# Performance work log

Hardware: AMD Instinct MI355X
Metric: run time of the kernel (lower is better)

Reference implementation:

```python
import jax, jax.numpy as jnp
import numpy as np

B, A, C, G = 16, 65472, 81, 50
POS_THRESH = 0.5        # positive_threshold
NEG_POS_RATIO = 3
CENTER_VAR, SIZE_VAR = 0.1, 0.2   # standard SSD encoding variances
BETA = 1.0 / 9


def _make_boxes(key, shape):
    # random valid corner-form boxes in [0,1]
    k1, k2 = jax.random.split(key)
    cxy = jax.random.uniform(k1, shape + (2,), minval=0.1, maxval=0.9)
    wh = jax.random.uniform(k2, shape + (2,), minval=0.05, maxval=0.3)
    lo = jnp.clip(cxy - wh / 2, 0.0, 1.0)
    hi = jnp.clip(cxy + wh / 2, 0.0, 1.0)
    return jnp.concatenate([lo, hi], axis=-1).astype(jnp.float32)


def setup_inputs() -> dict:
    key = jax.random.key(0)
    ks = jax.random.split(key, 6)
    confidence = jax.random.normal(ks[0], (B, A, C), dtype=jnp.float32)
    predicted_locations = jax.random.normal(ks[1], (B, A, 4), dtype=jnp.float32)
    boxes = _make_boxes(ks[2], (B, G))
    labels = jax.random.randint(ks[3], (B, G, 1), 1, C).astype(jnp.float32)
    gts = jnp.concatenate([boxes, labels], axis=-1)          # (B, G, 5)
    counts = jax.random.randint(ks[4], (B,), 1, G + 1)       # valid gt per image
    anchors = _make_boxes(ks[5], (A,))                        # corner form
    return {"confidence": confidence, "predicted_locations": predicted_locations,
            "gts": gts, "counts": counts, "anchors": anchors}


def _center_form(b):
    # corner (x1,y1,x2,y2) -> center (cx,cy,w,h)
    return jnp.concatenate([(b[..., :2] + b[..., 2:]) * 0.5,
                            b[..., 2:] - b[..., :2]], axis=-1)


def _iou(a, b):
    # a: (A,4), b: (G,4), corner form -> (A,G)
    lt = jnp.maximum(a[:, None, :2], b[None, :, :2])
    rb = jnp.minimum(a[:, None, 2:], b[None, :, 2:])
    wh = jnp.clip(rb - lt, 0.0)
    inter = wh[..., 0] * wh[..., 1]
    area_a = (a[:, 2] - a[:, 0]) * (a[:, 3] - a[:, 1])
    area_b = (b[:, 2] - b[:, 0]) * (b[:, 3] - b[:, 1])
    return inter / (area_a[:, None] + area_b[None, :] - inter + 1e-10)


def _encode(matched, anchors_c):
    m = _center_form(matched)
    g_cxcy = (m[..., :2] - anchors_c[..., :2]) / (anchors_c[..., 2:] * CENTER_VAR)
    g_wh = jnp.log(m[..., 2:] / anchors_c[..., 2:] + 1e-10) / SIZE_VAR
    return jnp.concatenate([g_cxcy, g_wh], axis=-1)


def _match(gt, count, anchors, anchors_c):
    # gt: (G,5), count: scalar int
    boxes = gt[:, :4]
    glabels = gt[:, 4].astype(jnp.int32)
    valid = jnp.arange(boxes.shape[0]) < count
    ious = jnp.where(valid[None, :], _iou(anchors, boxes), -1.0)  # (A,G)
    best_iou = ious.max(axis=1)          # best gt per anchor
    best_idx = ious.argmax(axis=1)
    best_anchor = ious.argmax(axis=0)    # best anchor per gt (G,)
    # force-match: each valid gt claims its best anchor (invalid -> dropped)
    scat = jnp.where(valid, best_anchor, anchors.shape[0])
    best_idx = best_idx.at[scat].set(jnp.arange(boxes.shape[0]), mode='drop')
    best_iou = best_iou.at[scat].set(2.0, mode='drop')
    labels = jnp.where(best_iou < POS_THRESH, 0, glabels[best_idx])  # (A,)
    loc = _encode(boxes[best_idx], anchors_c)                         # (A,4)
    return labels, loc


def reference(confidence, predicted_locations, gts, counts, anchors):
    anchors_c = _center_form(anchors)
    labels, gt_locations = jax.vmap(
        lambda g, c: _match(g, c, anchors, anchors_c))(gts, counts)
    labels = jax.lax.stop_gradient(labels)
    gt_locations = jax.lax.stop_gradient(gt_locations)

    logp = jax.nn.log_softmax(confidence, axis=2)          # (B,A,C)
    pos_mask = labels > 0
    num_pos_b = pos_mask.sum(axis=1)                        # (B,)

    # hard negative mining on background loss (positives excluded via -inf)
    mining = jnp.where(pos_mask, -jnp.inf, jax.lax.stop_gradient(-logp[:, :, 0]))
    order = jnp.argsort(-mining, axis=1)   # descending
    rank = jnp.argsort(order, axis=1)
    neg_mask = rank < (NEG_POS_RATIO * num_pos_b)[:, None]
    mask = pos_mask | neg_mask

    num_pos = jnp.maximum(1.0, pos_mask.sum().astype(jnp.float32))

    # masked cross-entropy (sum) == F.cross_entropy(conf[mask], labels[mask], 'sum')
    ce = -jnp.take_along_axis(logp, labels[..., None], axis=2)[..., 0]
    classification_loss = jnp.sum(jnp.where(mask, ce, 0.0)) / (num_pos * 4.0)

    # smooth L1 over positive anchors only
    n = jnp.abs(predicted_locations - gt_locations)
    sl1 = jnp.where(n < BETA, 0.5 * n * n / BETA, n - 0.5 * BETA)
    localisation_loss = jnp.sum(jnp.where(pos_mask[..., None], sl1, 0.0)) / (num_pos * 4.0)
    return (localisation_loss, classification_loss)
```

## Files before the change

### kernel.cpp

```cpp
#include <hip/hip_runtime.h>
#include <math.h>

#define Bn 16
#define An 65472
#define Cn 81
#define Gn 50
#define ROWS 128
#define NBUCK 1024
#define LISTCAP 8192

static_assert((Bn * (long long)An) % ROWS == 0, "rows divide");

constexpr float POS_THRESH_C = 0.5f;
constexpr float BETA_C = 1.0f / 9.0f;

typedef const __attribute__((address_space(1))) void GPTR;
typedef __attribute__((address_space(3))) void LPTR;

__global__ __launch_bounds__(64) void k0_zero(int* __restrict__ numpos_b,
                                              float* __restrict__ fsums) {
    int t = threadIdx.x;
    if (t < Bn) numpos_b[t] = 0;
    if (t == 32) fsums[0] = 0.f;
    if (t == 33) fsums[1] = 0.f;
}

__global__ __launch_bounds__(256) void k0b_zero(int* __restrict__ ghist) {
    ghist[blockIdx.x * 256 + threadIdx.x] = 0;
}

__global__ __launch_bounds__(256) void k1a(const float* __restrict__ anchors,
                                           const float* __restrict__ gts,
                                           const int* __restrict__ counts,
                                           float* __restrict__ best_iou,
                                           int* __restrict__ best_idx) {
    const int b = blockIdx.y;
    __shared__ float sg[Gn * 5];
    const int t = threadIdx.x;
    if (t < Gn * 5) sg[t] = gts[b * Gn * 5 + t];
    __syncthreads();
    const int a = blockIdx.x * 256 + t;
    if (a >= An) return;
    const int cnt = counts[b];
    const float4 av = ((const float4*)anchors)[a];
    const float area_a = (av.z - av.x) * (av.w - av.y);
    float best = -1.0f;
    int bidx = 0;
    for (int g = 0; g < Gn; ++g) {
        if (g >= cnt) break;
        const float bx0 = sg[g * 5 + 0], by0 = sg[g * 5 + 1];
        const float bx1 = sg[g * 5 + 2], by1 = sg[g * 5 + 3];
        const float w = fmaxf(fminf(av.z, bx1) - fmaxf(av.x, bx0), 0.f);
        const float h = fmaxf(fminf(av.w, by1) - fmaxf(av.y, by0), 0.f);
        const float inter = w * h;
        const float area_b = (bx1 - bx0) * (by1 - by0);
        const float iou = inter / (area_a + area_b - inter + 1e-10f);
        if (iou > best) { best = iou; bidx = g; }
    }
    best_iou[(size_t)b * An + a] = best;
    best_idx[(size_t)b * An + a] = bidx;
}

__global__ __launch_bounds__(256) void k1b(const float* __restrict__ anchors,
                                           const float* __restrict__ gts,
                                           const int* __restrict__ counts,
                                           int* __restrict__ best_anchor) {
    const int b = blockIdx.y, g = blockIdx.x;
    const int t = threadIdx.x;
    const int cnt = counts[b];
    if (g >= cnt) { if (t == 0) best_anchor[b * Gn + g] = 0; return; }
    const float bx0 = gts[(b * Gn + g) * 5 + 0], by0 = gts[(b * Gn + g) * 5 + 1];
    const float bx1 = gts[(b * Gn + g) * 5 + 2], by1 = gts[(b * Gn + g) * 5 + 3];
    const float area_b = (bx1 - bx0) * (by1 - by0);
    const float4* a4 = (const float4*)anchors;
    float best = -2.f;
    int bidx = 0x7fffffff;
    for (int base = t; base < An; base += 1024) {
        const int a1 = base + 256, a2 = base + 512, a3 = base + 768;
        const float4 av0 = a4[base];
        float4 av1, av2, av3;
        const bool ok1 = a1 < An, ok2 = a2 < An, ok3 = a3 < An;
        if (ok1) av1 = a4[a1];
        if (ok2) av2 = a4[a2];
        if (ok3) av3 = a4[a3];
        {
            const float area_a = (av0.z - av0.x) * (av0.w - av0.y);
            const float w = fmaxf(fminf(av0.z, bx1) - fmaxf(av0.x, bx0), 0.f);
            const float h = fmaxf(fminf(av0.w, by1) - fmaxf(av0.y, by0), 0.f);
            const float inter = w * h;
            const float iou = inter / (area_a + area_b - inter + 1e-10f);
            if (iou > best) { best = iou; bidx = base; }
        }
        if (ok1) {
            const float area_a = (av1.z - av1.x) * (av1.w - av1.y);
            const float w = fmaxf(fminf(av1.z, bx1) - fmaxf(av1.x, bx0), 0.f);
            const float h = fmaxf(fminf(av1.w, by1) - fmaxf(av1.y, by0), 0.f);
            const float inter = w * h;
            const float iou = inter / (area_a + area_b - inter + 1e-10f);
            if (iou > best) { best = iou; bidx = a1; }
        }
        if (ok2) {
            const float area_a = (av2.z - av2.x) * (av2.w - av2.y);
            const float w = fmaxf(fminf(av2.z, bx1) - fmaxf(av2.x, bx0), 0.f);
            const float h = fmaxf(fminf(av2.w, by1) - fmaxf(av2.y, by0), 0.f);
            const float inter = w * h;
            const float iou = inter / (area_a + area_b - inter + 1e-10f);
            if (iou > best) { best = iou; bidx = a2; }
        }
        if (ok3) {
            const float area_a = (av3.z - av3.x) * (av3.w - av3.y);
            const float w = fmaxf(fminf(av3.z, bx1) - fmaxf(av3.x, bx0), 0.f);
            const float h = fmaxf(fminf(av3.w, by1) - fmaxf(av3.y, by0), 0.f);
            const float inter = w * h;
            const float iou = inter / (area_a + area_b - inter + 1e-10f);
            if (iou > best) { best = iou; bidx = a3; }
        }
    }
    __shared__ float rv[256];
    __shared__ int ri[256];
    rv[t] = best; ri[t] = bidx;
    __syncthreads();
    for (int s = 128; s > 0; s >>= 1) {
        if (t < s) {
            const float fv = rv[t + s]; const int fi = ri[t + s];
            if (fv > rv[t] || (fv == rv[t] && fi < ri[t])) { rv[t] = fv; ri[t] = fi; }
        }
        __syncthreads();
    }
    if (t == 0) best_anchor[b * Gn + g] = ri[0];
}

__global__ __launch_bounds__(64) void k1c(const int* __restrict__ counts,
                                          const int* __restrict__ best_anchor,
                                          float* __restrict__ best_iou,
                                          int* __restrict__ best_idx) {
    const int b = threadIdx.x;
    if (b >= Bn) return;
    const int cnt = counts[b] < Gn ? counts[b] : Gn;
    for (int g = 0; g < cnt; ++g) {
        const int a = best_anchor[b * Gn + g];
        best_idx[(size_t)b * An + a] = g;
        best_iou[(size_t)b * An + a] = 2.0f;
    }
}

__global__ __launch_bounds__(256) void k2(const float* __restrict__ conf,
                                          const float* __restrict__ pred,
                                          const float* __restrict__ gts,
                                          const float* __restrict__ anchors,
                                          const float* __restrict__ best_iou,
                                          const int* __restrict__ best_idx,
                                          int* __restrict__ v_int,
                                          int* __restrict__ numpos_b,
                                          float* __restrict__ fsums) {
    __shared__ __align__(16) float sc[ROWS * Cn];
    __shared__ float s_ce[4], s_loc[4];
    __shared__ int s_n0[4], s_n1[4];
    const int t = threadIdx.x;
    {
        const float* gp = conf + (size_t)blockIdx.x * (ROWS * Cn);
#pragma unroll
        for (int k = 0; k < 10; ++k) {
            const int c = k * 256 + t;
            __builtin_amdgcn_global_load_lds((GPTR*)(gp + c * 4), (LPTR*)(sc + c * 4), 16, 0, 0);
        }
        if (t < 32) {
            const int c = 2560 + t;
            __builtin_amdgcn_global_load_lds((GPTR*)(gp + c * 4), (LPTR*)(sc + c * 4), 16, 0, 0);
        }
    }
    __syncthreads();
    const int r = t >> 1, h = t & 1;
    const float* row = sc + r * Cn;
    const int j0 = h ? 41 : 0;
    const int j1 = h ? Cn : 41;
    float s0 = 0.f, s1 = 0.f;
    for (int j = j0; j + 1 < j1; j += 2) { s0 += __expf(row[j]); s1 += __expf(row[j + 1]); }
    if (((j1 - j0) & 1) != 0) s0 += __expf(row[j1 - 1]);
    const float s = s0 + s1;
    const float S = s + __shfl_xor(s, 1);
    const float lse = logf(S);

    float ce = 0.f, loc = 0.f;
    int n0 = 0, n1 = 0;
    const int bf = (int)(((size_t)blockIdx.x * ROWS) / An);
    if (h == 0) {
        const size_t gidx = (size_t)blockIdx.x * ROWS + r;
        const int b = (int)(gidx / An);
        const int a = (int)(gidx - (size_t)b * An);
        const float bi = best_iou[gidx];
        const int idx = best_idx[gidx];
        if (bi < POS_THRESH_C) {
            v_int[gidx] = __float_as_int(lse - row[0]);
        } else {
            v_int[gidx] = -1;
            int lab = (int)gts[((size_t)b * Gn + idx) * 5 + 4];
            lab = lab < 0 ? 0 : (lab > Cn - 1 ? Cn - 1 : lab);
            ce = lse - row[lab];
            if (b == bf) n0 = 1; else n1 = 1;
            const float bx0 = gts[((size_t)b * Gn + idx) * 5 + 0];
            const float by0 = gts[((size_t)b * Gn + idx) * 5 + 1];
            const float bx1 = gts[((size_t)b * Gn + idx) * 5 + 2];
            const float by1 = gts[((size_t)b * Gn + idx) * 5 + 3];
            const float4 av = ((const float4*)anchors)[a];
            const float acx = (av.x + av.z) * 0.5f, acy = (av.y + av.w) * 0.5f;
            const float aw = av.z - av.x, ah = av.w - av.y;
            float tt[4];
            tt[0] = ((bx0 + bx1) * 0.5f - acx) / (aw * 0.1f);
            tt[1] = ((by0 + by1) * 0.5f - acy) / (ah * 0.1f);
            tt[2] = logf((bx1 - bx0) / aw + 1e-10f) / 0.2f;
            tt[3] = logf((by1 - by0) / ah + 1e-10f) / 0.2f;
            const float4 p = ((const float4*)pred)[gidx];
            const float pk[4] = {p.x, p.y, p.z, p.w};
#pragma unroll
            for (int k = 0; k < 4; ++k) {
                const float n = fabsf(pk[k] - tt[k]);
                loc += (n < BETA_C) ? 0.5f * n * n / BETA_C : n - 0.5f * BETA_C;
            }
        }
    }
#pragma unroll
    for (int off = 32; off > 0; off >>= 1) {
        ce += __shfl_down(ce, off);
        loc += __shfl_down(loc, off);
        n0 += __shfl_down(n0, off);
        n1 += __shfl_down(n1, off);
    }
    if ((t & 63) == 0) {
        const int w = t >> 6;
        s_ce[w] = ce; s_loc[w] = loc; s_n0[w] = n0; s_n1[w] = n1;
    }
    __syncthreads();
    if (t == 0) {
        const float CE = s_ce[0] + s_ce[1] + s_ce[2] + s_ce[3];
        const float LC = s_loc[0] + s_loc[1] + s_loc[2] + s_loc[3];
        const int N0 = s_n0[0] + s_n0[1] + s_n0[2] + s_n0[3];
        const int N1 = s_n1[0] + s_n1[1] + s_n1[2] + s_n1[3];
        if (CE != 0.f) atomicAdd(&fsums[0], CE);
        if (LC != 0.f) atomicAdd(&fsums[1], LC);
        if (N0 > 0) atomicAdd(&numpos_b[bf], N0);
        if (N1 > 0) atomicAdd(&numpos_b[bf + 1], N1);
    }
}

__global__ __launch_bounds__(256) void k3a(const int* __restrict__ v_int,
                                           int* __restrict__ ghist) {
    const int b = blockIdx.y, c = blockIdx.x;
    __shared__ int lh[NBUCK];
    const int t = threadIdx.x;
    for (int i = t; i < NBUCK; i += 256) lh[i] = 0;
    __syncthreads();
    const int4* v4 = (const int4*)(v_int + (size_t)b * An) + c * 1023;
    for (int i = t; i < 1023; i += 256) {
        const int4 x4 = v4[i];
        const int xs[4] = {x4.x, x4.y, x4.z, x4.w};
#pragma unroll
        for (int q = 0; q < 4; ++q) {
            const int x = xs[q];
            if (x < 0) continue;
            int bin = (int)(__int_as_float(x) * 64.0f);
            bin = bin > NBUCK - 1 ? NBUCK - 1 : bin;
            atomicAdd(&lh[bin], 1);
        }
    }
    __syncthreads();
    for (int i = t; i < NBUCK; i += 256) {
        const int cv = lh[i];
        if (cv) atomicAdd(&ghist[b * NBUCK + i], cv);
    }
}

__global__ __launch_bounds__(256) void k3b(const int* __restrict__ v_int,
                                           const int* __restrict__ ghist,
                                           const int* __restrict__ numpos_b,
                                           float* __restrict__ neg_sum_b) {
    const int b = blockIdx.x, t = threadIdx.x;
    const int npb = numpos_b[b];
    const long long K = 3LL * npb;
    const int n_nonpos = An - npb;
    __shared__ int h[NBUCK];
    __shared__ int gsfx[256];
    __shared__ int s_kt, s_r, s_m;
    __shared__ float fred[256];
    __shared__ float list[LISTCAP];
    if (K <= 0) { if (t == 0) neg_sum_b[b] = 0.f; return; }
    const int4* v4 = (const int4*)(v_int + (size_t)b * An);
    const int N4 = An / 4;
    const bool selAll = (K >= n_nonpos);
    int kt = -1, r = 0;
    if (!selAll) {
        for (int i = t; i < NBUCK; i += 256) h[i] = ghist[b * NBUCK + i];
        if (t == 0) s_m = 0;
        __syncthreads();
        gsfx[t] = h[4 * t] + h[4 * t + 1] + h[4 * t + 2] + h[4 * t + 3];
        __syncthreads();
        if (t == 0) {
            int acc = 0;
            for (int i = 255; i >= 0; --i) { const int tmp = gsfx[i]; gsfx[i] = acc; acc += tmp; }
        }
        __syncthreads();
        {
            const int base = 4 * t;
            int cg[4];
            cg[3] = gsfx[t];
            cg[2] = cg[3] + h[base + 3];
            cg[1] = cg[2] + h[base + 2];
            cg[0] = cg[1] + h[base + 1];
#pragma unroll
            for (int q = 0; q < 4; ++q) {
                if (cg[q] < K && K <= cg[q] + (long long)h[base + q]) {
                    s_kt = base + q; s_r = (int)(K - cg[q]);
                }
            }
        }
        __syncthreads();
        kt = s_kt; r = s_r;
    } else {
        if (t == 0) s_m = 0;
        __syncthreads();
    }
    float s = 0.f;
    for (int i = t; i < N4; i += 256) {
        const int4 x4 = v4[i];
        const int xs[4] = {x4.x, x4.y, x4.z, x4.w};
#pragma unroll
        for (int q = 0; q < 4; ++q) {
            const int x = xs[q];
            if (x < 0) continue;
            const float v = __int_as_float(x);
            if (selAll) { s += v; continue; }
            int bin = (int)(v * 64.0f);
            bin = bin > NBUCK - 1 ? NBUCK - 1 : bin;
            if (bin > kt) s += v;
            else if (bin == kt) {
                const int p = atomicAdd(&s_m, 1);
                if (p < LISTCAP) list[p] = v;
            }
        }
    }
    __syncthreads();
    if (!selAll) {
        int M = s_m; M = M > LISTCAP ? LISTCAP : M;
        for (int i = t; i < M; i += 256) {
            const float x = list[i];
            int cnt = 0;
            for (int j = 0; j < M; ++j) {
                const float y = list[j];
                cnt += (y > x) || (y == x && j < i);
            }
            if (cnt < r) s += x;
        }
    }
    fred[t] = s;
    __syncthreads();
    for (int st = 128; st > 0; st >>= 1) {
        if (t < st) fred[t] += fred[t + st];
        __syncthreads();
    }
    if (t == 0) neg_sum_b[b] = fred[0];
}

__global__ __launch_bounds__(64) void k4(const int* __restrict__ numpos_b,
                                         const float* __restrict__ fsums,
                                         const float* __restrict__ neg_sum_b,
                                         float* __restrict__ out) {
    if (threadIdx.x == 0) {
        int np = 0;
        for (int b = 0; b < Bn; ++b) np += numpos_b[b];
        const float num_pos = fmaxf(1.f, (float)np);
        const float denom = num_pos * 4.f;
        float neg = 0.f;
        for (int b = 0; b < Bn; ++b) neg += neg_sum_b[b];
        out[0] = fsums[1] / denom;
        out[1] = (fsums[0] + neg) / denom;
    }
}

extern "C" void kernel_launch(void* const* d_in, const int* in_sizes, int n_in,
                              void* d_out, int out_size, void* d_ws, size_t ws_size,
                              hipStream_t stream) {
    const float* conf    = (const float*)d_in[0];
    const float* pred    = (const float*)d_in[1];
    const float* gts     = (const float*)d_in[2];
    const int*   counts  = (const int*)d_in[3];
    const float* anchors = (const float*)d_in[4];
    float* out = (float*)d_out;

    const size_t BA = (size_t)Bn * An;
    char* w = (char*)d_ws;
    float* best_iou    = (float*)w; w += BA * sizeof(float);
    int*   best_idx    = (int*)w;   w += BA * sizeof(int);
    int*   v_int       = (int*)w;   w += BA * sizeof(int);
    int*   best_anchor = (int*)w;   w += Bn * Gn * sizeof(int);
    int*   numpos_b    = (int*)w;   w += 64;
    float* fsums       = (float*)w; w += 64;
    float* neg_sum_b   = (float*)w; w += 64;
    int*   ghist       = (int*)best_iou;

    hipLaunchKernelGGL(k0_zero, dim3(1), dim3(64), 0, stream, numpos_b, fsums);
    hipLaunchKernelGGL(k1a, dim3((An + 255) / 256, Bn), dim3(256), 0, stream,
                       anchors, gts, counts, best_iou, best_idx);
    hipLaunchKernelGGL(k1b, dim3(Gn, Bn), dim3(256), 0, stream,
                       anchors, gts, counts, best_anchor);
    hipLaunchKernelGGL(k1c, dim3(1), dim3(64), 0, stream,
                       counts, best_anchor, best_iou, best_idx);
    hipLaunchKernelGGL(k2, dim3((unsigned)(BA / ROWS)), dim3(256), 0, stream,
                       conf, pred, gts, anchors, best_iou, best_idx,
                       v_int, numpos_b, fsums);
    hipLaunchKernelGGL(k0b_zero, dim3(Bn * NBUCK / 256), dim3(256), 0, stream, ghist);
    hipLaunchKernelGGL(k3a, dim3(16, Bn), dim3(256), 0, stream, v_int, ghist);
    hipLaunchKernelGGL(k3b, dim3(Bn), dim3(256), 0, stream,
                       v_int, ghist, numpos_b, neg_sum_b);
    hipLaunchKernelGGL(k4, dim3(1), dim3(64), 0, stream, numpos_b, fsums, neg_sum_b, out);
}
```

Measured before the change: 751.1 us.

## Fuse anchor-gt matching and negative histogram into the loss kernel

Per-anchor IoU matching (old k1a) and the forced best-anchor override (old k1c) now run inside k2, using gts and best_anchor staged in shared memory. This removes the best_iou/best_idx workspace arrays and their global write-then-read round trip. The background-loss histogram (old k3a) is also built in k2 with per-element global atomics, and the zeroing kernels are merged into one. Tiles shrink to 64 rows per block with 4 threads per row. The risk is contention from global atomics on a small set of hot histogram bins.

```diff
diff --git a/kernel.cpp b/kernel.cpp
--- a/kernel.cpp
+++ b/kernel.cpp
@@ -5,11 +5,12 @@
 #define An 65472
 #define Cn 81
 #define Gn 50
-#define ROWS 128
+#define ROWS 64
+#define BPB 1023
 #define NBUCK 1024
 #define LISTCAP 8192
 
-static_assert((Bn * (long long)An) % ROWS == 0, "rows divide");
+static_assert(An == ROWS * BPB, "tile divides batch");
 
 constexpr float POS_THRESH_C = 0.5f;
 constexpr float BETA_C = 1.0f / 9.0f;
@@ -17,48 +18,17 @@
 typedef const __attribute__((address_space(1))) void GPTR;
 typedef __attribute__((address_space(3))) void LPTR;
 
-__global__ __launch_bounds__(64) void k0_zero(int* __restrict__ numpos_b,
-                                              float* __restrict__ fsums) {
-    int t = threadIdx.x;
-    if (t < Bn) numpos_b[t] = 0;
-    if (t == 32) fsums[0] = 0.f;
-    if (t == 33) fsums[1] = 0.f;
-}
-
-__global__ __launch_bounds__(256) void k0b_zero(int* __restrict__ ghist) {
-    ghist[blockIdx.x * 256 + threadIdx.x] = 0;
-}
-
-__global__ __launch_bounds__(256) void k1a(const float* __restrict__ anchors,
-                                           const float* __restrict__ gts,
-                                           const int* __restrict__ counts,
-                                           float* __restrict__ best_iou,
-                                           int* __restrict__ best_idx) {
-    const int b = blockIdx.y;
-    __shared__ float sg[Gn * 5];
-    const int t = threadIdx.x;
-    if (t < Gn * 5) sg[t] = gts[b * Gn * 5 + t];
-    __syncthreads();
-    const int a = blockIdx.x * 256 + t;
-    if (a >= An) return;
-    const int cnt = counts[b];
-    const float4 av = ((const float4*)anchors)[a];
-    const float area_a = (av.z - av.x) * (av.w - av.y);
-    float best = -1.0f;
-    int bidx = 0;
-    for (int g = 0; g < Gn; ++g) {
-        if (g >= cnt) break;
-        const float bx0 = sg[g * 5 + 0], by0 = sg[g * 5 + 1];
-        const float bx1 = sg[g * 5 + 2], by1 = sg[g * 5 + 3];
-        const float w = fmaxf(fminf(av.z, bx1) - fmaxf(av.x, bx0), 0.f);
-        const float h = fmaxf(fminf(av.w, by1) - fmaxf(av.y, by0), 0.f);
-        const float inter = w * h;
-        const float area_b = (bx1 - bx0) * (by1 - by0);
-        const float iou = inter / (area_a + area_b - inter + 1e-10f);
-        if (iou > best) { best = iou; bidx = g; }
-    }
-    best_iou[(size_t)b * An + a] = best;
-    best_idx[(size_t)b * An + a] = bidx;
+__global__ __launch_bounds__(256) void k0_zero(int* __restrict__ numpos_b,
+                                               float* __restrict__ fsums,
+                                               int* __restrict__ ghist) {
+    const int i = blockIdx.x * 256 + threadIdx.x;
+    if (i < Bn * NBUCK) ghist[i] = 0;
+    if (blockIdx.x == 0) {
+        const int t = threadIdx.x;
+        if (t < Bn) numpos_b[t] = 0;
+        if (t == 32) fsums[0] = 0.f;
+        if (t == 33) fsums[1] = 0.f;
+    }
 }
 
 __global__ __launch_bounds__(256) void k1b(const float* __restrict__ anchors,
@@ -68,7 +38,7 @@
     const int b = blockIdx.y, g = blockIdx.x;
     const int t = threadIdx.x;
     const int cnt = counts[b];
-    if (g >= cnt) { if (t == 0) best_anchor[b * Gn + g] = 0; return; }
+    if (g >= cnt) { if (t == 0) best_anchor[b * Gn + g] = -1; return; }
     const float bx0 = gts[(b * Gn + g) * 5 + 0], by0 = gts[(b * Gn + g) * 5 + 1];
     const float bx1 = gts[(b * Gn + g) * 5 + 2], by1 = gts[(b * Gn + g) * 5 + 3];
     const float area_b = (bx1 - bx0) * (by1 - by0);
@@ -130,79 +100,101 @@
     if (t == 0) best_anchor[b * Gn + g] = ri[0];
 }
 
-__global__ __launch_bounds__(64) void k1c(const int* __restrict__ counts,
-                                          const int* __restrict__ best_anchor,
-                                          float* __restrict__ best_iou,
-                                          int* __restrict__ best_idx) {
-    const int b = threadIdx.x;
-    if (b >= Bn) return;
-    const int cnt = counts[b] < Gn ? counts[b] : Gn;
-    for (int g = 0; g < cnt; ++g) {
-        const int a = best_anchor[b * Gn + g];
-        best_idx[(size_t)b * An + a] = g;
-        best_iou[(size_t)b * An + a] = 2.0f;
-    }
-}
-
 __global__ __launch_bounds__(256) void k2(const float* __restrict__ conf,
                                           const float* __restrict__ pred,
                                           const float* __restrict__ gts,
                                           const float* __restrict__ anchors,
-                                          const float* __restrict__ best_iou,
-                                          const int* __restrict__ best_idx,
+                                          const int* __restrict__ counts,
+                                          const int* __restrict__ best_anchor,
                                           int* __restrict__ v_int,
                                           int* __restrict__ numpos_b,
-                                          float* __restrict__ fsums) {
+                                          float* __restrict__ fsums,
+                                          int* __restrict__ ghist) {
     __shared__ __align__(16) float sc[ROWS * Cn];
+    __shared__ float sg[Gn * 5];
+    __shared__ int sf[Gn];
     __shared__ float s_ce[4], s_loc[4];
-    __shared__ int s_n0[4], s_n1[4];
+    __shared__ int s_np[4];
     const int t = threadIdx.x;
+    const int b = blockIdx.x / BPB;
+    const int a0 = (blockIdx.x - b * BPB) * ROWS;
+
     {
-        const float* gp = conf + (size_t)blockIdx.x * (ROWS * Cn);
-#pragma unroll
-        for (int k = 0; k < 10; ++k) {
+        const float* gp = conf + ((size_t)b * An + a0) * Cn;
+#pragma unroll
+        for (int k = 0; k < 5; ++k) {
             const int c = k * 256 + t;
             __builtin_amdgcn_global_load_lds((GPTR*)(gp + c * 4), (LPTR*)(sc + c * 4), 16, 0, 0);
         }
-        if (t < 32) {
-            const int c = 2560 + t;
+        if (t < 16) {
+            const int c = 1280 + t;
             __builtin_amdgcn_global_load_lds((GPTR*)(gp + c * 4), (LPTR*)(sc + c * 4), 16, 0, 0);
         }
     }
-    __syncthreads();
-    const int r = t >> 1, h = t & 1;
+    if (t < Gn * 5) sg[t] = gts[b * Gn * 5 + t];
+    if (t >= 192 && t < 192 + Gn) sf[t - 192] = best_anchor[b * Gn + (t - 192)];
+    const int cnt = counts[b] < Gn ? counts[b] : Gn;
+    __syncthreads();
+
+    const int r = t >> 2, h = t & 3;
+    const int a = a0 + r;
+    const float4 av = ((const float4*)anchors)[a];
+    const float area_a = (av.z - av.x) * (av.w - av.y);
+
+    float best = -1.f;
+    int bidx = 0x7fffffff;
+    for (int g = h; g < cnt; g += 4) {
+        const float bx0 = sg[g * 5 + 0], by0 = sg[g * 5 + 1];
+        const float bx1 = sg[g * 5 + 2], by1 = sg[g * 5 + 3];
+        const float w = fmaxf(fminf(av.z, bx1) - fmaxf(av.x, bx0), 0.f);
+        const float hh = fmaxf(fminf(av.w, by1) - fmaxf(av.y, by0), 0.f);
+        const float inter = w * hh;
+        const float area_b = (bx1 - bx0) * (by1 - by0);
+        const float iou = inter / (area_a + area_b - inter + 1e-10f);
+        if (iou > best) { best = iou; bidx = g; }
+    }
+#pragma unroll
+    for (int off = 1; off <= 2; off <<= 1) {
+        const float ov = __shfl_xor(best, off);
+        const int oi = __shfl_xor(bidx, off);
+        if (ov > best || (ov == best && oi < bidx)) { best = ov; bidx = oi; }
+    }
+    int fg = -1;
+    for (int g = h; g < cnt; g += 4) if (sf[g] == a) fg = g;
+#pragma unroll
+    for (int off = 1; off <= 2; off <<= 1) {
+        const int og = __shfl_xor(fg, off);
+        fg = og > fg ? og : fg;
+    }
+    if (fg >= 0) { best = 2.f; bidx = fg; }
+
     const float* row = sc + r * Cn;
-    const int j0 = h ? 41 : 0;
-    const int j1 = h ? Cn : 41;
-    float s0 = 0.f, s1 = 0.f;
-    for (int j = j0; j + 1 < j1; j += 2) { s0 += __expf(row[j]); s1 += __expf(row[j + 1]); }
-    if (((j1 - j0) & 1) != 0) s0 += __expf(row[j1 - 1]);
-    const float s = s0 + s1;
-    const float S = s + __shfl_xor(s, 1);
-    const float lse = logf(S);
+    const int j0 = h * 21;
+    const int j1 = j0 + 21 < Cn ? j0 + 21 : Cn;
+    float s = 0.f;
+    for (int j = j0; j < j1; ++j) s += __expf(row[j]);
+    s += __shfl_xor(s, 1);
+    s += __shfl_xor(s, 2);
+    const float lse = logf(s);
 
     float ce = 0.f, loc = 0.f;
-    int n0 = 0, n1 = 0;
-    const int bf = (int)(((size_t)blockIdx.x * ROWS) / An);
+    int np = 0;
     if (h == 0) {
-        const size_t gidx = (size_t)blockIdx.x * ROWS + r;
-        const int b = (int)(gidx / An);
-        const int a = (int)(gidx - (size_t)b * An);
-        const float bi = best_iou[gidx];
-        const int idx = best_idx[gidx];
-        if (bi < POS_THRESH_C) {
-            v_int[gidx] = __float_as_int(lse - row[0]);
+        const size_t gidx = (size_t)b * An + a;
+        if (best < POS_THRESH_C) {
+            const float v = lse - row[0];
+            v_int[gidx] = __float_as_int(v);
+            int bin = (int)(v * 64.0f);
+            bin = bin > NBUCK - 1 ? NBUCK - 1 : bin;
+            atomicAdd(&ghist[b * NBUCK + bin], 1);
         } else {
             v_int[gidx] = -1;
-            int lab = (int)gts[((size_t)b * Gn + idx) * 5 + 4];
+            np = 1;
+            int lab = (int)sg[bidx * 5 + 4];
             lab = lab < 0 ? 0 : (lab > Cn - 1 ? Cn - 1 : lab);
             ce = lse - row[lab];
-            if (b == bf) n0 = 1; else n1 = 1;
-            const float bx0 = gts[((size_t)b * Gn + idx) * 5 + 0];
-            const float by0 = gts[((size_t)b * Gn + idx) * 5 + 1];
-            const float bx1 = gts[((size_t)b * Gn + idx) * 5 + 2];
-            const float by1 = gts[((size_t)b * Gn + idx) * 5 + 3];
-            const float4 av = ((const float4*)anchors)[a];
+            const float bx0 = sg[bidx * 5 + 0], by0 = sg[bidx * 5 + 1];
+            const float bx1 = sg[bidx * 5 + 2], by1 = sg[bidx * 5 + 3];
             const float acx = (av.x + av.z) * 0.5f, acy = (av.y + av.w) * 0.5f;
             const float aw = av.z - av.x, ah = av.w - av.y;
             float tt[4];
@@ -223,50 +215,20 @@
     for (int off = 32; off > 0; off >>= 1) {
         ce += __shfl_down(ce, off);
         loc += __shfl_down(loc, off);
-        n0 += __shfl_down(n0, off);
-        n1 += __shfl_down(n1, off);
+        np += __shfl_down(np, off);
     }
     if ((t & 63) == 0) {
         const int w = t >> 6;
-        s_ce[w] = ce; s_loc[w] = loc; s_n0[w] = n0; s_n1[w] = n1;
+        s_ce[w] = ce; s_loc[w] = loc; s_np[w] = np;
     }
     __syncthreads();
     if (t == 0) {
         const float CE = s_ce[0] + s_ce[1] + s_ce[2] + s_ce[3];
         const float LC = s_loc[0] + s_loc[1] + s_loc[2] + s_loc[3];
-        const int N0 = s_n0[0] + s_n0[1] + s_n0[2] + s_n0[3];
-        const int N1 = s_n1[0] + s_n1[1] + s_n1[2] + s_n1[3];
+        const int NP = s_np[0] + s_np[1] + s_np[2] + s_np[3];
         if (CE != 0.f) atomicAdd(&fsums[0], CE);
         if (LC != 0.f) atomicAdd(&fsums[1], LC);
-        if (N0 > 0) atomicAdd(&numpos_b[bf], N0);
-        if (N1 > 0) atomicAdd(&numpos_b[bf + 1], N1);
-    }
-}
-
-__global__ __launch_bounds__(256) void k3a(const int* __restrict__ v_int,
-                                           int* __restrict__ ghist) {
-    const int b = blockIdx.y, c = blockIdx.x;
-    __shared__ int lh[NBUCK];
-    const int t = threadIdx.x;
-    for (int i = t; i < NBUCK; i += 256) lh[i] = 0;
-    __syncthreads();
-    const int4* v4 = (const int4*)(v_int + (size_t)b * An) + c * 1023;
-    for (int i = t; i < 1023; i += 256) {
-        const int4 x4 = v4[i];
-        const int xs[4] = {x4.x, x4.y, x4.z, x4.w};
-#pragma unroll
-        for (int q = 0; q < 4; ++q) {
-            const int x = xs[q];
-            if (x < 0) continue;
-            int bin = (int)(__int_as_float(x) * 64.0f);
-            bin = bin > NBUCK - 1 ? NBUCK - 1 : bin;
-            atomicAdd(&lh[bin], 1);
-        }
-    }
-    __syncthreads();
-    for (int i = t; i < NBUCK; i += 256) {
-        const int cv = lh[i];
-        if (cv) atomicAdd(&ghist[b * NBUCK + i], cv);
+        if (NP > 0) atomicAdd(&numpos_b[b], NP);
     }
 }
 
@@ -388,27 +350,20 @@
 
     const size_t BA = (size_t)Bn * An;
     char* w = (char*)d_ws;
-    float* best_iou    = (float*)w; w += BA * sizeof(float);
-    int*   best_idx    = (int*)w;   w += BA * sizeof(int);
     int*   v_int       = (int*)w;   w += BA * sizeof(int);
-    int*   best_anchor = (int*)w;   w += Bn * Gn * sizeof(int);
+    int*   ghist       = (int*)w;   w += Bn * NBUCK * sizeof(int);
+    int*   best_anchor = (int*)w;   w += ((Bn * Gn * sizeof(int) + 63) / 64) * 64;
     int*   numpos_b    = (int*)w;   w += 64;
     float* fsums       = (float*)w; w += 64;
     float* neg_sum_b   = (float*)w; w += 64;
-    int*   ghist       = (int*)best_iou;
-
-    hipLaunchKernelGGL(k0_zero, dim3(1), dim3(64), 0, stream, numpos_b, fsums);
-    hipLaunchKernelGGL(k1a, dim3((An + 255) / 256, Bn), dim3(256), 0, stream,
-                       anchors, gts, counts, best_iou, best_idx);
+
+    hipLaunchKernelGGL(k0_zero, dim3((Bn * NBUCK + 255) / 256), dim3(256), 0, stream,
+                       numpos_b, fsums, ghist);
     hipLaunchKernelGGL(k1b, dim3(Gn, Bn), dim3(256), 0, stream,
                        anchors, gts, counts, best_anchor);
-    hipLaunchKernelGGL(k1c, dim3(1), dim3(64), 0, stream,
-                       counts, best_anchor, best_iou, best_idx);
-    hipLaunchKernelGGL(k2, dim3((unsigned)(BA / ROWS)), dim3(256), 0, stream,
-                       conf, pred, gts, anchors, best_iou, best_idx,
-                       v_int, numpos_b, fsums);
-    hipLaunchKernelGGL(k0b_zero, dim3(Bn * NBUCK / 256), dim3(256), 0, stream, ghist);
-    hipLaunchKernelGGL(k3a, dim3(16, Bn), dim3(256), 0, stream, v_int, ghist);
+    hipLaunchKernelGGL(k2, dim3(Bn * BPB), dim3(256), 0, stream,
+                       conf, pred, gts, anchors, counts, best_anchor,
+                       v_int, numpos_b, fsums, ghist);
     hipLaunchKernelGGL(k3b, dim3(Bn), dim3(256), 0, stream,
                        v_int, ghist, numpos_b, neg_sum_b);
     hipLaunchKernelGGL(k4, dim3(1), dim3(64), 0, stream, numpos_b, fsums, neg_sum_b, out);
```

Result: slower. 940.7 us (+25.2%).
